# Optimization experiments

Measured on AMD Instinct MI355X. Metric: run time of the kernel, lower is better.

Reference implementation:

```python
import jax, jax.numpy as jnp
import numpy as np
from jax import lax


def _conv(x, w, b, stride, pad):
    # x: NCHW, w: OIHW (pytorch Conv2d layout)
    y = lax.conv_general_dilated(x, w, window_strides=(stride, stride),
                                 padding=((pad, pad), (pad, pad)),
                                 dimension_numbers=('NCHW', 'OIHW', 'NCHW'))
    return y + b[None, :, None, None]


def _deconv(x, w, b):
    # PyTorch ConvTranspose2d(k=4, stride=2, padding=1); w: [in, out, 4, 4]
    # Equivalent to conv with lhs_dilation=2, padding k-1-p=2, flipped/transposed kernel.
    wk = jnp.flip(w, (2, 3)).transpose(1, 0, 2, 3)  # -> OIHW
    y = lax.conv_general_dilated(x, wk, window_strides=(1, 1),
                                 padding=((2, 2), (2, 2)), lhs_dilation=(2, 2),
                                 dimension_numbers=('NCHW', 'OIHW', 'NCHW'))
    return y + b[None, :, None, None]


def _mse(a, b):
    d = a - b
    return jnp.mean(d * d)


def _forward(x, enc_w1, enc_b1, enc_w2, enc_b2, enc_w3, enc_b3, codebook,
             dec_w1, dec_b1, dec_w2, dec_b2, dec_w3, dec_b3, beta=0.25):
    # ---- Encoder ----
    h = jax.nn.relu(_conv(x, enc_w1, enc_b1, 2, 1))
    h = jax.nn.relu(_conv(h, enc_w2, enc_b2, 2, 1))
    z_e = _conv(h, enc_w3, enc_b3, 1, 1)            # [B, D, H, W]
    B, D, H, W = z_e.shape

    # ---- Vector quantize ----
    z_flat = z_e.transpose(0, 2, 3, 1).reshape(-1, D)              # [N, D]
    dist = (jnp.sum(z_flat * z_flat, axis=1, keepdims=True)
            + jnp.sum(codebook * codebook, axis=1)
            - 2.0 * z_flat @ codebook.T)                            # [N, K]
    idx = jnp.argmin(dist, axis=1)                                  # [N]
    z_q = codebook[idx].reshape(B, H, W, D).transpose(0, 3, 1, 2)   # [B, D, H, W]

    commitment_loss = beta * _mse(lax.stop_gradient(z_e), z_q)
    codebook_loss = _mse(z_e, lax.stop_gradient(z_q))
    vq_loss = codebook_loss + commitment_loss
    z_q_st = z_e + lax.stop_gradient(z_q - z_e)     # straight-through

    # ---- Decoder ----
    d1 = jax.nn.relu(_deconv(z_q_st, dec_w1, dec_b1))
    d2 = jax.nn.relu(_deconv(d1, dec_w2, dec_b2))
    x_recon = _conv(d2, dec_w3, dec_b3, 1, 1)

    recon_loss = _mse(x_recon, x)
    total_loss = recon_loss + vq_loss
    return x_recon, total_loss, recon_loss, vq_loss


def setup_inputs() -> dict:
    key = jax.random.key(0)
    ks = jax.random.split(key, 16)
    s = 0.05
    K, D, Hc = 512, 64, 128
    return {
        'x':       jax.random.normal(ks[0], (64, 3, 128, 128), jnp.float32),
        'enc_w1':  jax.random.normal(ks[1], (Hc, 3, 4, 4), jnp.float32) * s,
        'enc_b1':  jnp.zeros((Hc,), jnp.float32),
        'enc_w2':  jax.random.normal(ks[2], (Hc, Hc, 4, 4), jnp.float32) * s,
        'enc_b2':  jnp.zeros((Hc,), jnp.float32),
        'enc_w3':  jax.random.normal(ks[3], (D, Hc, 3, 3), jnp.float32) * s,
        'enc_b3':  jnp.zeros((D,), jnp.float32),
        'codebook': jax.random.uniform(ks[4], (K, D), jnp.float32, -1.0 / K, 1.0 / K),
        'dec_w1':  jax.random.normal(ks[5], (D, Hc, 4, 4), jnp.float32) * s,  # ConvTranspose [in,out,k,k]
        'dec_b1':  jnp.zeros((Hc,), jnp.float32),
        'dec_w2':  jax.random.normal(ks[6], (Hc, Hc, 4, 4), jnp.float32) * s,
        'dec_b2':  jnp.zeros((Hc,), jnp.float32),
        'dec_w3':  jax.random.normal(ks[7], (3, Hc, 3, 3), jnp.float32) * s,
        'dec_b3':  jnp.zeros((3,), jnp.float32),
    }


def reference(x, enc_w1, enc_b1, enc_w2, enc_b2, enc_w3, enc_b3, codebook,
              dec_w1, dec_b1, dec_w2, dec_b2, dec_w3, dec_b3):
    return _forward(x, enc_w1, enc_b1, enc_w2, enc_b2, enc_w3, enc_b3, codebook,
                    dec_w1, dec_b1, dec_w2, dec_b2, dec_w3, dec_b3)
```

## Files before the change

### kernel.cpp

```cpp
#include <hip/hip_runtime.h>
#include <hip/hip_bf16.h>


typedef __attribute__((ext_vector_type(8))) short short8;
typedef __attribute__((ext_vector_type(16))) float f32x16;
typedef __attribute__((ext_vector_type(4))) float f32x4;

__device__ __forceinline__ unsigned short f2bf(float f) {
  union { __hip_bfloat16 b; unsigned short u; } cv;
  cv.b = __float2bfloat16(f);
  return cv.u;
}
__device__ __forceinline__ unsigned pack2bf(float a, float b) {
  return (unsigned)f2bf(a) | ((unsigned)f2bf(b) << 16);
}

template<int CI, int NTAP, int NTALL>
__global__ void repack_conv_w(const float* __restrict__ w,
                              unsigned short* __restrict__ wb, int co_real) {
  const int KC = CI / 16;
  const int total = NTAP * KC * NTALL * 512;
  int i = blockIdx.x * 256 + threadIdx.x;
  if (i >= total) return;
  int j = i & 7, lane = (i >> 3) & 63, t2 = i >> 9;
  int nt = t2 % NTALL; t2 /= NTALL;
  int kc = t2 % KC; int tap = t2 / KC;
  int co = nt * 32 + (lane & 31);
  int ci = kc * 16 + (lane >> 5) * 8 + j;
  float v = (co < co_real) ? w[(co * CI + ci) * NTAP + tap] : 0.f;
  wb[i] = f2bf(v);
}

template<int CI, int CO, int NTALL>
__global__ void repack_deconv_w(const float* __restrict__ w,
                                unsigned short* __restrict__ wb) {
  const int KC = CI / 16;
  const int total = 16 * KC * NTALL * 512;
  int i = blockIdx.x * 256 + threadIdx.x;
  if (i >= total) return;
  int j = i & 7, lane = (i >> 3) & 63, t2 = i >> 9;
  int nt = t2 % NTALL; t2 /= NTALL;
  int kc = t2 % KC; t2 /= KC;
  int tap = t2 & 3, cls = t2 >> 2;
  int a = cls >> 1, b = cls & 1, ti = tap >> 1, tj = tap & 1;
  int kh = 2 * ti + 1 - a, kw = 2 * tj + 1 - b;
  int co = nt * 32 + (lane & 31);
  int ci = kc * 16 + (lane >> 5) * 8 + j;
  wb[i] = f2bf(w[((ci * CO + co) * 4 + kh) * 4 + kw]);
}

__global__ void repack_conv4_w(const float* __restrict__ w,
                               unsigned short* __restrict__ wb) {
  const int total = 9 * 4 * 512;
  int i = blockIdx.x * 256 + threadIdx.x;
  if (i >= total) return;
  int j = i & 7, lane = (i >> 3) & 63, tk = i >> 9;
  int kc = tk & 3, t = tk >> 2;
  int co = lane & 15;
  int ci = kc * 32 + (lane >> 4) * 8 + j;
  float v = (co < 3) ? w[(co * 128 + ci) * 9 + t] : 0.f;
  wb[i] = f2bf(v);
}

__global__ void repack_conv1_w(const float* __restrict__ w,
                               float* __restrict__ wc1) {
  int i = blockIdx.x * 256 + threadIdx.x;
  if (i >= 6144) return;
  int tap = i >> 7, co = i & 127;
  wc1[i] = w[co * 48 + tap];
}

__global__ void repack_cb(const float* __restrict__ cb,
                          unsigned short* __restrict__ cbf) {
  int i = blockIdx.x * 256 + threadIdx.x;
  int j = i & 7, lane = (i >> 3) & 63;
  int kc = (i >> 9) & 3, tile = i >> 11;
  int code = tile * 32 + (lane & 31);
  int d = kc * 16 + (lane >> 5) * 8 + j;
  cbf[i] = f2bf(cb[code * 64 + d]);
}
__global__ void cnorm_k(const float* __restrict__ cb, float* __restrict__ cn) {
  int k = blockIdx.x * 256 + threadIdx.x;
  if (k >= 512) return;
  const float4* r = (const float4*)(cb + k * 64);
  float s = 0.f;
  #pragma unroll
  for (int q = 0; q < 16; ++q) {
    float4 v = r[q];
    s = fmaf(v.x, v.x, s); s = fmaf(v.y, v.y, s);
    s = fmaf(v.z, v.z, s); s = fmaf(v.w, v.w, s);
  }
  cn[k] = s;
}

__global__ __launch_bounds__(256, 4) void conv1_k(
    const float* __restrict__ x, const float* __restrict__ wc1,
    const float* __restrict__ bias, unsigned short* __restrict__ out) {
  __shared__ float swc[6144];
  __shared__ float sx[3 * 10 * 132];
  int tid = threadIdx.x;
  int n = blockIdx.x >> 4, ohq = blockIdx.x & 15;
  #pragma unroll
  for (int q = 0; q < 6; ++q) {
    int i = (q * 256 + tid) * 4;
    *(float4*)&swc[i] = *(const float4*)&wc1[i];
  }
  int ihb = 8 * ohq - 1;
  for (int i = tid; i < 3960; i += 256) {
    int ci = i / 1320, rem = i - ci * 1320;
    int r = rem / 132, c = rem - r * 132;
    int ih = ihb + r, iw = c - 1;
    float v = 0.f;
    if ((unsigned)ih < 128u && (unsigned)iw < 128u)
      v = x[(n * 3 + ci) * 16384 + ih * 128 + iw];
    sx[i] = v;
  }
  __syncthreads();
  int ow = tid >> 2, cg = tid & 3;
  #pragma unroll
  for (int cob = 0; cob < 2; ++cob) {
    int co0 = cob * 64 + cg * 16;
    float4 acc[4][4];
    float4 bq[4];
    #pragma unroll
    for (int q = 0; q < 4; ++q) bq[q] = *(const float4*)&bias[co0 + q * 4];
    #pragma unroll
    for (int o = 0; o < 4; ++o)
      #pragma unroll
      for (int q = 0; q < 4; ++q) acc[o][q] = bq[q];
    for (int ci = 0; ci < 3; ++ci)
      for (int kh = 0; kh < 4; ++kh) {
        #pragma unroll
        for (int kw = 0; kw < 4; ++kw) {
          int tap = ci * 16 + kh * 4 + kw;
          const float* wp = &swc[tap * 128 + co0];
          float4 w0 = *(const float4*)(wp);
          float4 w1 = *(const float4*)(wp + 4);
          float4 w2 = *(const float4*)(wp + 8);
          float4 w3 = *(const float4*)(wp + 12);
          const float* xp = &sx[ci * 1320 + kh * 132 + 2 * ow + kw];
          #pragma unroll
          for (int o = 0; o < 4; ++o) {
            float xv = xp[o * 264];
            acc[o][0].x = fmaf(xv, w0.x, acc[o][0].x);
            acc[o][0].y = fmaf(xv, w0.y, acc[o][0].y);
            acc[o][0].z = fmaf(xv, w0.z, acc[o][0].z);
            acc[o][0].w = fmaf(xv, w0.w, acc[o][0].w);
            acc[o][1].x = fmaf(xv, w1.x, acc[o][1].x);
            acc[o][1].y = fmaf(xv, w1.y, acc[o][1].y);
            acc[o][1].z = fmaf(xv, w1.z, acc[o][1].z);
            acc[o][1].w = fmaf(xv, w1.w, acc[o][1].w);
            acc[o][2].x = fmaf(xv, w2.x, acc[o][2].x);
            acc[o][2].y = fmaf(xv, w2.y, acc[o][2].y);
            acc[o][2].z = fmaf(xv, w2.z, acc[o][2].z);
            acc[o][2].w = fmaf(xv, w2.w, acc[o][2].w);
            acc[o][3].x = fmaf(xv, w3.x, acc[o][3].x);
            acc[o][3].y = fmaf(xv, w3.y, acc[o][3].y);
            acc[o][3].z = fmaf(xv, w3.z, acc[o][3].z);
            acc[o][3].w = fmaf(xv, w3.w, acc[o][3].w);
          }
        }
      }
    #pragma unroll
    for (int o = 0; o < 4; ++o) {
      int oh = ohq * 4 + o;
      unsigned short* op = out + ((size_t)(n * 64 + oh) * 64 + ow) * 128 + co0;
      uint4 u0, u1;
      u0.x = pack2bf(fmaxf(acc[o][0].x, 0.f), fmaxf(acc[o][0].y, 0.f));
      u0.y = pack2bf(fmaxf(acc[o][0].z, 0.f), fmaxf(acc[o][0].w, 0.f));
      u0.z = pack2bf(fmaxf(acc[o][1].x, 0.f), fmaxf(acc[o][1].y, 0.f));
      u0.w = pack2bf(fmaxf(acc[o][1].z, 0.f), fmaxf(acc[o][1].w, 0.f));
      u1.x = pack2bf(fmaxf(acc[o][2].x, 0.f), fmaxf(acc[o][2].y, 0.f));
      u1.y = pack2bf(fmaxf(acc[o][2].z, 0.f), fmaxf(acc[o][2].w, 0.f));
      u1.z = pack2bf(fmaxf(acc[o][3].x, 0.f), fmaxf(acc[o][3].y, 0.f));
      u1.w = pack2bf(fmaxf(acc[o][3].z, 0.f), fmaxf(acc[o][3].w, 0.f));
      *(uint4*)(op) = u0;
      *(uint4*)(op + 8) = u1;
    }
  }
}

template<int CI, int CO, int NTALL, int NT, int S, int IH, int IW, int OH, int OW,
         int NTAP, int KW, int STRIDE, bool DECONV, bool RELU, bool F32OUT>
__global__ __launch_bounds__(256, 4) void mconv_k(
    const unsigned short* __restrict__ in, const unsigned short* __restrict__ wb,
    const float* __restrict__ bias, void* __restrict__ outv,
    const unsigned short* __restrict__ zeropg) {
  const int KC = CI / 16;
  const int TSZ = KC * NT * 512;
  const int STG = KC * NT / 4;
  __shared__ unsigned short sB[2][TSZ];
  int tid = threadIdx.x, lane = tid & 63, wv = tid >> 6;
  int m0 = blockIdx.x * (128 * S) + wv * (32 * S);
  int cls = DECONV ? blockIdx.y : 0;
  int cog = blockIdx.z;
  int ca = cls >> 1, cb2 = cls & 1;
  int khalf = lane >> 5;
  int n_[S], oh_[S], ow_[S];
  #pragma unroll
  for (int s = 0; s < S; ++s) {
    int mm = m0 + s * 32 + (lane & 31);
    n_[s] = mm / (OH * OW);
    int rem = mm % (OH * OW);
    oh_[s] = rem / OW; ow_[s] = rem % OW;
  }
  f32x16 acc[S][NT];
  #pragma unroll
  for (int s = 0; s < S; ++s)
    #pragma unroll
    for (int t = 0; t < NT; ++t)
      #pragma unroll
      for (int e = 0; e < 16; ++e) acc[s][t][e] = 0.f;

  const unsigned short* wcls = wb + (size_t)cls * NTAP * KC * NTALL * 512;
  uint4 st[STG];
  #pragma unroll
  for (int q = 0; q < STG; ++q) {
    int i = q * 256 + tid;
    int kc = i / (NT * 64), r = i - kc * (NT * 64);
    st[q] = *(const uint4*)(wcls + (size_t)(kc * NTALL + cog * NT) * 512 + r * 8);
  }
  #pragma unroll
  for (int q = 0; q < STG; ++q) {
    int i = q * 256 + tid;
    *(uint4*)&sB[0][i * 8] = st[q];
  }
  __syncthreads();

  for (int t = 0; t < NTAP; ++t) {
    int cur = t & 1;
    if (t + 1 < NTAP) {
      const unsigned short* wt = wcls + (size_t)(t + 1) * KC * NTALL * 512;
      #pragma unroll
      for (int q = 0; q < STG; ++q) {
        int i = q * 256 + tid;
        int kc = i / (NT * 64), r = i - kc * (NT * 64);
        st[q] = *(const uint4*)(wt + (size_t)(kc * NTALL + cog * NT) * 512 + r * 8);
      }
    }
    const unsigned short* ap[S];
    #pragma unroll
    for (int s = 0; s < S; ++s) {
      int ih, iw;
      if (DECONV) { ih = oh_[s] + ca - (t >> 1); iw = ow_[s] + cb2 - (t & 1); }
      else        { ih = STRIDE * oh_[s] - 1 + t / KW; iw = STRIDE * ow_[s] - 1 + t % KW; }
      bool valid = ((unsigned)ih < (unsigned)IH) && ((unsigned)iw < (unsigned)IW);
      ap[s] = valid ? (in + ((size_t)(n_[s] * IH + ih) * IW + iw) * CI + khalf * 8)
                    : (zeropg + khalf * 8);
    }
    #pragma unroll
    for (int kc = 0; kc < KC; ++kc) {
      short8 a[S];
      #pragma unroll
      for (int s = 0; s < S; ++s) a[s] = *(const short8*)(ap[s] + kc * 16);
      #pragma unroll
      for (int nt = 0; nt < NT; ++nt) {
        short8 b = *(const short8*)&sB[cur][(kc * NT + nt) * 512 + lane * 8];
        #pragma unroll
        for (int s = 0; s < S; ++s)
          acc[s][nt] = __builtin_amdgcn_mfma_f32_32x32x16_bf16(a[s], b, acc[s][nt], 0, 0, 0);
      }
    }
    if (t + 1 < NTAP) {
      #pragma unroll
      for (int q = 0; q < STG; ++q) {
        int i = q * 256 + tid;
        *(uint4*)&sB[cur ^ 1][i * 8] = st[q];
      }
    }
    __syncthreads();
  }

  int col = lane & 31;
  #pragma unroll
  for (int s = 0; s < S; ++s)
    #pragma unroll
    for (int nt = 0; nt < NT; ++nt) {
      int co = (cog * NT + nt) * 32 + col;
      float bv = bias[co];
      #pragma unroll
      for (int r = 0; r < 16; ++r) {
        int mrow = (r & 3) + 8 * (r >> 2) + 4 * khalf;
        int mp = m0 + s * 32 + mrow;
        int n2 = mp / (OH * OW), r2 = mp % (OH * OW);
        int oh2 = r2 / OW, ow2 = r2 % OW;
        float v = acc[s][nt][r] + bv;
        if (RELU) v = fmaxf(v, 0.f);
        size_t idx;
        if (DECONV)
          idx = ((size_t)(n2 * (2 * OH) + 2 * oh2 + ca) * (2 * OW) + 2 * ow2 + cb2) * CO + co;
        else
          idx = ((size_t)(n2 * OH + oh2) * OW + ow2) * CO + co;
        if (F32OUT) ((float*)outv)[idx] = v;
        else        ((unsigned short*)outv)[idx] = f2bf(v);
      }
    }
}

__global__ __launch_bounds__(256, 2) void vq2_k(
    const float* __restrict__ ze, const float* __restrict__ cb,
    const unsigned short* __restrict__ cbf, const float* __restrict__ cnorm,
    unsigned short* __restrict__ zq, float* __restrict__ acc_loss) {
  __shared__ unsigned short sC[16384];
  __shared__ int s_idx[4][32];
  int tid = threadIdx.x, lane = tid & 63, wv = tid >> 6;
  int m0 = blockIdx.x * 128 + wv * 32;
  int col = lane & 31, khalf = lane >> 5;
  const float* zrow = ze + (size_t)(m0 + col) * 64 + khalf * 8;
  short8 af[4];
  #pragma unroll
  for (int kc = 0; kc < 4; ++kc) {
    float4 a = *(const float4*)(zrow + kc * 16);
    float4 b = *(const float4*)(zrow + kc * 16 + 4);
    short8 f;
    f[0] = (short)f2bf(a.x); f[1] = (short)f2bf(a.y);
    f[2] = (short)f2bf(a.z); f[3] = (short)f2bf(a.w);
    f[4] = (short)f2bf(b.x); f[5] = (short)f2bf(b.y);
    f[6] = (short)f2bf(b.z); f[7] = (short)f2bf(b.w);
    af[kc] = f;
  }
  float best[16]; int bidx[16];
  #pragma unroll
  for (int r = 0; r < 16; ++r) { best[r] = 3.4e38f; bidx[r] = 0; }
  for (int half = 0; half < 2; ++half) {
    #pragma unroll
    for (int q = 0; q < 8; ++q) {
      int i = q * 256 + tid;
      *(uint4*)&sC[i * 8] = *(const uint4*)(cbf + half * 16384 + i * 8);
    }
    __syncthreads();
    #pragma unroll
    for (int t8 = 0; t8 < 8; ++t8) {
      int tt = half * 8 + t8;
      f32x16 acc;
      #pragma unroll
      for (int e = 0; e < 16; ++e) acc[e] = 0.f;
      #pragma unroll
      for (int kc = 0; kc < 4; ++kc) {
        short8 bf_ = *(const short8*)&sC[(t8 * 4 + kc) * 512 + lane * 8];
        acc = __builtin_amdgcn_mfma_f32_32x32x16_bf16(af[kc], bf_, acc, 0, 0, 0);
      }
      float cn = cnorm[tt * 32 + col];
      int code = tt * 32 + col;
      #pragma unroll
      for (int r = 0; r < 16; ++r) {
        float d = fmaf(-2.f, acc[r], cn);
        if (d < best[r]) { best[r] = d; bidx[r] = code; }
      }
    }
    __syncthreads();
  }
  #pragma unroll
  for (int off = 1; off < 32; off <<= 1) {
    #pragma unroll
    for (int r = 0; r < 16; ++r) {
      float ob = __shfl_xor(best[r], off, 64);
      int   oi = __shfl_xor(bidx[r], off, 64);
      if (ob < best[r]) { best[r] = ob; bidx[r] = oi; }
    }
  }
  if (col == 0) {
    #pragma unroll
    for (int r = 0; r < 16; ++r)
      s_idx[wv][(r & 3) + 8 * (r >> 2) + 4 * khalf] = bidx[r];
  }
  __syncthreads();
  int row = lane >> 1, half2 = lane & 1;
  int m = m0 + row;
  int idx = s_idx[wv][row];
  const float4* crow = (const float4*)(cb + idx * 64 + half2 * 32);
  const float4* zp = (const float4*)(ze + (size_t)m * 64 + half2 * 32);
  uint2* zqp = (uint2*)(zq + (size_t)m * 64 + half2 * 32);
  float lsum = 0.f;
  #pragma unroll
  for (int q = 0; q < 8; ++q) {
    float4 c4 = crow[q];
    float4 z4 = zp[q];
    uint2 u; u.x = pack2bf(c4.x, c4.y); u.y = pack2bf(c4.z, c4.w);
    zqp[q] = u;
    float d;
    d = z4.x - c4.x; lsum = fmaf(d, d, lsum);
    d = z4.y - c4.y; lsum = fmaf(d, d, lsum);
    d = z4.z - c4.z; lsum = fmaf(d, d, lsum);
    d = z4.w - c4.w; lsum = fmaf(d, d, lsum);
  }
  #pragma unroll
  for (int off = 32; off > 0; off >>= 1) lsum += __shfl_down(lsum, off, 64);
  if (lane == 0) atomicAdd(acc_loss, lsum);
}

__global__ __launch_bounds__(256, 4) void conv4_k(
    const unsigned short* __restrict__ in, const unsigned short* __restrict__ wb,
    const float* __restrict__ bias, const float* __restrict__ x,
    float* __restrict__ out, float* __restrict__ acc_loss,
    const unsigned short* __restrict__ zeropg) {
  __shared__ unsigned short sW[18432];
  int tid = threadIdx.x, lane = tid & 63, wv = tid >> 6;
  #pragma unroll
  for (int q = 0; q < 9; ++q) {
    int i = q * 256 + tid;
    *(uint4*)&sW[i * 8] = *(const uint4*)(wb + i * 8);
  }
  int m0 = blockIdx.x * 256 + wv * 64;
  int quad = lane >> 4, mloc = lane & 15;
  int n_[4], oh_[4], ow_[4];
  #pragma unroll
  for (int s = 0; s < 4; ++s) {
    int mm = m0 + s * 16 + mloc;
    n_[s] = mm >> 14;
    int rem = mm & 16383;
    oh_[s] = rem >> 7; ow_[s] = rem & 127;
  }
  f32x4 acc[4];
  #pragma unroll
  for (int s = 0; s < 4; ++s)
    #pragma unroll
    for (int e = 0; e < 4; ++e) acc[s][e] = 0.f;
  __syncthreads();
  #pragma unroll
  for (int t = 0; t < 9; ++t) {
    int dh = t / 3 - 1, dw = t % 3 - 1;
    const unsigned short* ap[4];
    #pragma unroll
    for (int s = 0; s < 4; ++s) {
      int ih = oh_[s] + dh, iw = ow_[s] + dw;
      bool valid = ((unsigned)ih < 128u) && ((unsigned)iw < 128u);
      ap[s] = valid ? (in + ((size_t)(n_[s] * 128 + ih) * 128 + iw) * 128 + quad * 8)
                    : (zeropg + quad * 8);
    }
    #pragma unroll
    for (int kc = 0; kc < 4; ++kc) {
      short8 bf_ = *(const short8*)&sW[(t * 4 + kc) * 512 + lane * 8];
      #pragma unroll
      for (int s = 0; s < 4; ++s) {
        short8 a = *(const short8*)(ap[s] + kc * 32);
        acc[s] = __builtin_amdgcn_mfma_f32_16x16x32_bf16(a, bf_, acc[s], 0, 0, 0);
      }
    }
  }
  int co = lane & 15;
  float bv = (co < 3) ? bias[co] : 0.f;
  float lsum = 0.f;
  #pragma unroll
  for (int s = 0; s < 4; ++s)
    #pragma unroll
    for (int r = 0; r < 4; ++r) {
      int m = m0 + s * 16 + quad * 4 + r;
      if (co < 3) {
        float v = acc[s][r] + bv;
        int n2 = m >> 14, r2 = m & 16383;
        int gi = (n2 * 3 + co) * 16384 + r2;
        out[gi] = v;
        float d = v - x[gi];
        lsum = fmaf(d, d, lsum);
      }
    }
  #pragma unroll
  for (int off = 32; off > 0; off >>= 1) lsum += __shfl_down(lsum, off, 64);
  if (lane == 0) atomicAdd(acc_loss, lsum);
}

__global__ void finalize_k(const float* __restrict__ accv, float* __restrict__ out) {
  if (threadIdx.x == 0 && blockIdx.x == 0) {
    float recon = accv[0] / 3145728.0f;
    float vq = 1.25f * accv[1] / 4194304.0f;
    out[3145728] = recon + vq;
    out[3145729] = recon;
    out[3145730] = vq;
  }
}

extern "C" void kernel_launch(void* const* d_in, const int* in_sizes, int n_in,
                              void* d_out, int out_size, void* d_ws, size_t ws_size,
                              hipStream_t stream) {
  const float* x   = (const float*)d_in[0];
  const float* ew1 = (const float*)d_in[1];
  const float* eb1 = (const float*)d_in[2];
  const float* ew2 = (const float*)d_in[3];
  const float* eb2 = (const float*)d_in[4];
  const float* ew3 = (const float*)d_in[5];
  const float* eb3 = (const float*)d_in[6];
  const float* cb  = (const float*)d_in[7];
  const float* dw1 = (const float*)d_in[8];
  const float* db1 = (const float*)d_in[9];
  const float* dw2 = (const float*)d_in[10];
  const float* db2 = (const float*)d_in[11];
  const float* dw3 = (const float*)d_in[12];
  const float* db3 = (const float*)d_in[13];
  float* out = (float*)d_out;

  char* ws = (char*)d_ws;
  float* acc = (float*)ws;
  unsigned short* zeropg = (unsigned short*)(ws + 256);
  char* p = ws + 1024;
  unsigned short* wb2  = (unsigned short*)p; p += 524288;
  unsigned short* wb3  = (unsigned short*)p; p += 147456;
  unsigned short* wb4  = (unsigned short*)p; p += 36864;
  unsigned short* wbd1 = (unsigned short*)p; p += 262144;
  unsigned short* wbd2 = (unsigned short*)p; p += 524288;
  unsigned short* cbf  = (unsigned short*)p; p += 65536;
  float*          cnrm = (float*)p;          p += 2048;
  float*          wc1  = (float*)p;          p += 24576;
  size_t fixed = (size_t)(p - ws);

  unsigned short* h1 = (unsigned short*)p; p += 67108864ull;
  unsigned short* h2 = (unsigned short*)p; p += 16777216ull;
  float*          ze = (float*)p;          p += 16777216ull;
  unsigned short* zq = (unsigned short*)p; p += 8388608ull;
  unsigned short* d2 = (unsigned short*)p;
  size_t base = fixed + 67108864ull + 16777216ull + 16777216ull + 8388608ull;
  int CD = 64;
  while (CD > 1 && base + (size_t)CD * 4194304ull > ws_size) CD >>= 1;

  hipMemsetAsync(ws, 0, 1024, stream);
  repack_conv_w<128, 16, 4><<<(16 * 8 * 4 * 512 + 255) / 256, 256, 0, stream>>>(ew2, wb2, 128);
  repack_conv_w<128, 9, 2><<<(9 * 8 * 2 * 512 + 255) / 256, 256, 0, stream>>>(ew3, wb3, 64);
  repack_conv4_w<<<(9 * 4 * 512 + 255) / 256, 256, 0, stream>>>(dw3, wb4);
  repack_deconv_w<64, 128, 4><<<(16 * 4 * 4 * 512 + 255) / 256, 256, 0, stream>>>(dw1, wbd1);
  repack_deconv_w<128, 128, 4><<<(16 * 8 * 4 * 512 + 255) / 256, 256, 0, stream>>>(dw2, wbd2);
  repack_cb<<<128, 256, 0, stream>>>(cb, cbf);
  cnorm_k<<<2, 256, 0, stream>>>(cb, cnrm);
  repack_conv1_w<<<24, 256, 0, stream>>>(ew1, wc1);

  conv1_k<<<1024, 256, 0, stream>>>(x, wc1, eb1, h1);
  mconv_k<128, 128, 4, 2, 2, 64, 64, 32, 32, 16, 4, 2, false, true, false>
      <<<dim3(256, 1, 2), 256, 0, stream>>>(h1, wb2, eb2, h2, zeropg);
  mconv_k<128, 64, 2, 2, 2, 32, 32, 32, 32, 9, 3, 1, false, false, true>
      <<<dim3(256, 1, 1), 256, 0, stream>>>(h2, wb3, eb3, ze, zeropg);
  vq2_k<<<512, 256, 0, stream>>>(ze, cb, cbf, cnrm, zq, acc + 1);
  mconv_k<64, 128, 4, 2, 2, 32, 32, 32, 32, 4, 2, 1, true, true, false>
      <<<dim3(256, 4, 2), 256, 0, stream>>>(zq, wbd1, db1, h1, zeropg);

  for (int n0 = 0; n0 < 64; n0 += CD) {
    const unsigned short* d1c = h1 + (size_t)n0 * 524288;
    mconv_k<128, 128, 4, 2, 2, 64, 64, 64, 64, 4, 2, 1, true, true, false>
        <<<dim3(CD * 16, 4, 2), 256, 0, stream>>>(d1c, wbd2, db2, d2, zeropg);
    conv4_k<<<CD * 64, 256, 0, stream>>>(d2, wb4, db3, x + (size_t)n0 * 49152,
                                         out + (size_t)n0 * 49152, acc, zeropg);
  }
  finalize_k<<<1, 64, 0, stream>>>(acc, out);
}
```

Baseline: 1.106 ms.

## Add specialized deconv kernel with precomputed tap pointers and reorder conv4 loops

Replaces the generic mconv_k for both transposed-conv decoder layers with a dedicated dconv_k. It precomputes all four tap input pointers up front and loads only this block's output-channel slice of the weights into shared memory. conv4_k now also precomputes the nine tap pointers and swaps the loop order to kc-outer, tap-inner, with launch bounds lowered from 4 to 3 blocks. The aim is to cut per-iteration address arithmetic and expose more independent loads; holding more pointers raises register pressure and may reduce occupancy.

```diff
diff --git a/kernel.cpp b/kernel.cpp
--- a/kernel.cpp
+++ b/kernel.cpp
@@ -297,6 +297,93 @@
     }
 }
 
+template<int CI, int CO, int NTALL, int NT, int S, int HW>
+__global__ __launch_bounds__(256, 2) void dconv_k(
+    const unsigned short* __restrict__ in, const unsigned short* __restrict__ wb,
+    const float* __restrict__ bias, unsigned short* __restrict__ out,
+    const unsigned short* __restrict__ zeropg) {
+  const int KC = CI / 16;
+  const int TOT = 4 * KC * NT * 512;
+  const int NU  = TOT / (8 * 256);
+  const int CHU = NT * 64;
+  __shared__ unsigned short sB[TOT];
+  int tid = threadIdx.x, lane = tid & 63, wv = tid >> 6;
+  int m0 = blockIdx.x * (128 * S) + wv * (32 * S);
+  int cls = blockIdx.y, cog = blockIdx.z;
+  int ca = cls >> 1, cb2 = cls & 1;
+  int khalf = lane >> 5;
+  int n_[S], oh_[S], ow_[S];
+  #pragma unroll
+  for (int s = 0; s < S; ++s) {
+    int mm = m0 + s * 32 + (lane & 31);
+    n_[s] = mm / (HW * HW);
+    int rem = mm % (HW * HW);
+    oh_[s] = rem / HW; ow_[s] = rem % HW;
+  }
+  const unsigned short* wcls = wb + (size_t)cls * 4 * KC * NTALL * 512;
+  #pragma unroll
+  for (int q = 0; q < NU; ++q) {
+    int g = q * 256 + tid;
+    int chunk = g / CHU, within = g - chunk * CHU;
+    *(uint4*)&sB[(chunk * NT * 64 + within) * 8] =
+        *(const uint4*)(wcls + ((size_t)chunk * NTALL + cog * NT) * 512 + within * 8);
+  }
+  const unsigned short* ap[4][S];
+  #pragma unroll
+  for (int t = 0; t < 4; ++t)
+    #pragma unroll
+    for (int s = 0; s < S; ++s) {
+      int ih = oh_[s] + ca - (t >> 1), iw = ow_[s] + cb2 - (t & 1);
+      bool valid = ((unsigned)ih < (unsigned)HW) && ((unsigned)iw < (unsigned)HW);
+      ap[t][s] = valid ? (in + ((size_t)(n_[s] * HW + ih) * HW + iw) * CI + khalf * 8)
+                       : (zeropg + khalf * 8);
+    }
+  f32x16 acc[S][NT];
+  #pragma unroll
+  for (int s = 0; s < S; ++s)
+    #pragma unroll
+    for (int t = 0; t < NT; ++t)
+      #pragma unroll
+      for (int e = 0; e < 16; ++e) acc[s][t][e] = 0.f;
+  __syncthreads();
+
+  #pragma unroll
+  for (int kc = 0; kc < KC; ++kc) {
+    #pragma unroll
+    for (int t = 0; t < 4; ++t) {
+      short8 a[S];
+      #pragma unroll
+      for (int s = 0; s < S; ++s) a[s] = *(const short8*)(ap[t][s] + kc * 16);
+      #pragma unroll
+      for (int nt = 0; nt < NT; ++nt) {
+        short8 b = *(const short8*)&sB[((t * KC + kc) * NT + nt) * 512 + lane * 8];
+        #pragma unroll
+        for (int s = 0; s < S; ++s)
+          acc[s][nt] = __builtin_amdgcn_mfma_f32_32x32x16_bf16(a[s], b, acc[s][nt], 0, 0, 0);
+      }
+    }
+  }
+
+  int col = lane & 31;
+  #pragma unroll
+  for (int s = 0; s < S; ++s)
+    #pragma unroll
+    for (int nt = 0; nt < NT; ++nt) {
+      int co = (cog * NT + nt) * 32 + col;
+      float bv = bias[co];
+      #pragma unroll
+      for (int r = 0; r < 16; ++r) {
+        int mrow = (r & 3) + 8 * (r >> 2) + 4 * khalf;
+        int mp = m0 + s * 32 + mrow;
+        int n2 = mp / (HW * HW), r2 = mp % (HW * HW);
+        int oh2 = r2 / HW, ow2 = r2 % HW;
+        float v = fmaxf(acc[s][nt][r] + bv, 0.f);
+        size_t idx = ((size_t)(n2 * (2 * HW) + 2 * oh2 + ca) * (2 * HW) + 2 * ow2 + cb2) * CO + co;
+        out[idx] = f2bf(v);
+      }
+    }
+}
+
 __global__ __launch_bounds__(256, 2) void vq2_k(
     const float* __restrict__ ze, const float* __restrict__ cb,
     const unsigned short* __restrict__ cbf, const float* __restrict__ cnorm,
@@ -389,7 +476,7 @@
   if (lane == 0) atomicAdd(acc_loss, lsum);
 }
 
-__global__ __launch_bounds__(256, 4) void conv4_k(
+__global__ __launch_bounds__(256, 3) void conv4_k(
     const unsigned short* __restrict__ in, const unsigned short* __restrict__ wb,
     const float* __restrict__ bias, const float* __restrict__ x,
     float* __restrict__ out, float* __restrict__ acc_loss,
@@ -411,29 +498,32 @@
     int rem = mm & 16383;
     oh_[s] = rem >> 7; ow_[s] = rem & 127;
   }
-  f32x4 acc[4];
-  #pragma unroll
-  for (int s = 0; s < 4; ++s)
-    #pragma unroll
-    for (int e = 0; e < 4; ++e) acc[s][e] = 0.f;
-  __syncthreads();
+  const unsigned short* ap[9][4];
   #pragma unroll
   for (int t = 0; t < 9; ++t) {
     int dh = t / 3 - 1, dw = t % 3 - 1;
-    const unsigned short* ap[4];
     #pragma unroll
     for (int s = 0; s < 4; ++s) {
       int ih = oh_[s] + dh, iw = ow_[s] + dw;
       bool valid = ((unsigned)ih < 128u) && ((unsigned)iw < 128u);
-      ap[s] = valid ? (in + ((size_t)(n_[s] * 128 + ih) * 128 + iw) * 128 + quad * 8)
-                    : (zeropg + quad * 8);
-    }
-    #pragma unroll
-    for (int kc = 0; kc < 4; ++kc) {
+      ap[t][s] = valid ? (in + ((size_t)(n_[s] * 128 + ih) * 128 + iw) * 128 + quad * 8)
+                       : (zeropg + quad * 8);
+    }
+  }
+  f32x4 acc[4];
+  #pragma unroll
+  for (int s = 0; s < 4; ++s)
+    #pragma unroll
+    for (int e = 0; e < 4; ++e) acc[s][e] = 0.f;
+  __syncthreads();
+  #pragma unroll
+  for (int kc = 0; kc < 4; ++kc) {
+    #pragma unroll
+    for (int t = 0; t < 9; ++t) {
       short8 bf_ = *(const short8*)&sW[(t * 4 + kc) * 512 + lane * 8];
       #pragma unroll
       for (int s = 0; s < 4; ++s) {
-        short8 a = *(const short8*)(ap[s] + kc * 32);
+        short8 a = *(const short8*)(ap[t][s] + kc * 32);
         acc[s] = __builtin_amdgcn_mfma_f32_16x16x32_bf16(a, bf_, acc[s], 0, 0, 0);
       }
     }
@@ -528,12 +618,12 @@
   mconv_k<128, 64, 2, 2, 2, 32, 32, 32, 32, 9, 3, 1, false, false, true>
       <<<dim3(256, 1, 1), 256, 0, stream>>>(h2, wb3, eb3, ze, zeropg);
   vq2_k<<<512, 256, 0, stream>>>(ze, cb, cbf, cnrm, zq, acc + 1);
-  mconv_k<64, 128, 4, 2, 2, 32, 32, 32, 32, 4, 2, 1, true, true, false>
+  dconv_k<64, 128, 4, 2, 2, 32>
       <<<dim3(256, 4, 2), 256, 0, stream>>>(zq, wbd1, db1, h1, zeropg);
 
   for (int n0 = 0; n0 < 64; n0 += CD) {
     const unsigned short* d1c = h1 + (size_t)n0 * 524288;
-    mconv_k<128, 128, 4, 2, 2, 64, 64, 64, 64, 4, 2, 1, true, true, false>
+    dconv_k<128, 128, 4, 2, 2, 64>
         <<<dim3(CD * 16, 4, 2), 256, 0, stream>>>(d1c, wbd2, db2, d2, zeropg);
     conv4_k<<<CD * 64, 256, 0, stream>>>(d2, wb4, db3, x + (size_t)n0 * 49152,
                                          out + (size_t)n0 * 49152, acc, zeropg);
```

Measured after the change: 1.138 ms. 1.03x slower.
